# Optimization experiments

Measured on AMD Instinct MI355X. Metric: run time of the kernel, lower is better.

Reference implementation:

```python
import jax, jax.numpy as jnp
import numpy as np

D_MODEL = 256
SCALE = 1.0 / float(np.sqrt(D_MODEL))


def setup_inputs() -> dict:
    key = jax.random.key(0)
    kq, kk, kv, km = jax.random.split(key, 4)
    B, S, D = 16, 2048, D_MODEL
    q = jax.random.normal(kq, (B, S, D), dtype=jnp.float32)
    k = jax.random.normal(kk, (B, S, D), dtype=jnp.float32)
    v = jax.random.normal(kv, (B, S, D), dtype=jnp.float32)
    mask = jax.random.randint(km, (1, S, S), 0, 2, dtype=jnp.int32)
    return {"q": q, "k": k, "v": v, "mask": mask}


def reference(q, k, v, mask):
    # scores: [B, S, S] = q @ k^T * scale
    scores = jnp.einsum("bqd,bkd->bqk", q, k) * SCALE
    scores = jnp.where(mask == 0, -jnp.inf, scores)
    attn_weights = jax.nn.softmax(scores, axis=-1)
    output = jnp.einsum("bqk,bkd->bqd", attn_weights, v)
    return (output, attn_weights)
```

## Files before the change

kernel.cpp:

```cpp
#include <hip/hip_runtime.h>
#include <hip/hip_bf16.h>
#include <stdint.h>


#define B_ 16
#define S_ 2048
#define D_ 256
#define SCALE_ 0.0625f

typedef __attribute__((ext_vector_type(8))) short bf16x8;
typedef __attribute__((ext_vector_type(4))) float f32x4;

__device__ __forceinline__ uint16_t f2bf(float f) {
  uint32_t u = __float_as_uint(f);
  u += 0x7fffu + ((u >> 16) & 1u);
  return (uint16_t)(u >> 16);
}

__global__ void k_convert(const float* __restrict__ src, uint16_t* __restrict__ dst) {
  const int t = blockIdx.x * blockDim.x + threadIdx.x;
  const float4* s = (const float4*)src + (size_t)t * 2;
  float4 a = s[0], b = s[1];
  ushort4 lo = { f2bf(a.x), f2bf(a.y), f2bf(a.z), f2bf(a.w) };
  ushort4 hi = { f2bf(b.x), f2bf(b.y), f2bf(b.z), f2bf(b.w) };
  ((ushort4*)dst)[(size_t)t * 2]     = lo;
  ((ushort4*)dst)[(size_t)t * 2 + 1] = hi;
}

__global__ void k_transpose(const float* __restrict__ V, uint16_t* __restrict__ Vt) {
  __shared__ float tile[64][68];
  const int b = blockIdx.z, kv0 = blockIdx.x * 64, d0 = blockIdx.y * 64;
  const int t = threadIdx.x;
  {
    const int r = t >> 2, c = (t & 3) * 16;
    const float4* src = (const float4*)(V + ((size_t)b * S_ + kv0 + r) * D_ + d0 + c);
    float4 x0 = src[0], x1 = src[1], x2 = src[2], x3 = src[3];
    *(float4*)&tile[r][c]      = x0;
    *(float4*)&tile[r][c + 4]  = x1;
    *(float4*)&tile[r][c + 8]  = x2;
    *(float4*)&tile[r][c + 12] = x3;
  }
  __syncthreads();
  {
    const int dl = t >> 2, c = (t & 3) * 16;
    uint16_t o[16];
#pragma unroll
    for (int i = 0; i < 16; ++i) o[i] = f2bf(tile[c + i][dl]);
    uint16_t* dst = Vt + ((size_t)b * D_ + d0 + dl) * S_ + kv0 + c;
#pragma unroll
    for (int i = 0; i < 4; ++i) {
      ushort4 v4 = { o[4*i], o[4*i+1], o[4*i+2], o[4*i+3] };
      *(ushort4*)(dst + 4*i) = v4;
    }
  }
}

__global__ void k_maskpack(const int* __restrict__ mask, unsigned long long* __restrict__ Mb) {
  const int wid  = blockIdx.x * 4 + (threadIdx.x >> 6);
  const int lane = threadIdx.x & 63;
  const int row = wid >> 5, w64 = wid & 31;
  const int m = mask[(size_t)row * S_ + w64 * 64 + lane];
  unsigned long long bits = __ballot(m != 0);
  if (lane == 0) Mb[row * 32 + w64] = bits;
}

__global__ __launch_bounds__(512, 2) void k_attn(
    const float* __restrict__ Q, const uint16_t* __restrict__ Kb,
    const unsigned long long* __restrict__ Mb, float* __restrict__ attn) {
  __shared__ uint16_t Ks[128 * 256];
  const int b = blockIdx.y, q0 = blockIdx.x * 128;
  const int tid = threadIdx.x, w = tid >> 6, lane = tid & 63;
  const int wq = w >> 1, wkv = w & 1;
  const int l15 = lane & 15, lq = lane >> 4;
  const int qbase = q0 + wq * 32;

  bf16x8 aq[2][8];
#pragma unroll
  for (int qt = 0; qt < 2; ++qt) {
    const float* qrow = Q + ((size_t)b * S_ + qbase + qt * 16 + l15) * D_;
#pragma unroll
    for (int dc = 0; dc < 8; ++dc) {
      const float4* p = (const float4*)(qrow + dc * 32 + lq * 8);
      float4 x = p[0], y = p[1];
      union { bf16x8 v; uint16_t u[8]; } fr;
      fr.u[0] = f2bf(x.x); fr.u[1] = f2bf(x.y); fr.u[2] = f2bf(x.z); fr.u[3] = f2bf(x.w);
      fr.u[4] = f2bf(y.x); fr.u[5] = f2bf(y.y); fr.u[6] = f2bf(y.z); fr.u[7] = f2bf(y.w);
      aq[qt][dc] = fr.v;
    }
  }

  float rowpart[2][4] = {{0.f,0.f,0.f,0.f},{0.f,0.f,0.f,0.f}};
  float inv_[2][4];

  for (int pass = 0; pass < 2; ++pass) {
    for (int kvt = 0; kvt < 16; ++kvt) {
      const int kvb = kvt * 128;
      {
        const uint4* src = (const uint4*)(Kb + ((size_t)b * S_ + kvb) * D_);
#pragma unroll
        for (int i = 0; i < 8; ++i) {
          const int g = i * 512 + tid;
          const int row = g >> 5, gcol = g & 31;
          uint4 val = src[row * 32 + gcol];
          const int gs = (gcol & ~7) | ((gcol ^ row) & 7);
          *(uint4*)&Ks[(row * 32 + gs) * 8] = val;
        }
      }
      __syncthreads();

      f32x4 acc[2][4];
#pragma unroll
      for (int qt = 0; qt < 2; ++qt)
#pragma unroll
        for (int kt = 0; kt < 4; ++kt) acc[qt][kt] = 0.f;

#pragma unroll
      for (int dc = 0; dc < 8; ++dc) {
        bf16x8 bk[4];
#pragma unroll
        for (int kt = 0; kt < 4; ++kt) {
          const int kvl = wkv * 64 + kt * 16 + l15;
          const int g = dc * 4 + lq;
          const int gs = (g & ~7) | ((g ^ kvl) & 7);
          bk[kt] = *(const bf16x8*)&Ks[(kvl * 32 + gs) * 8];
        }
#pragma unroll
        for (int qt = 0; qt < 2; ++qt)
#pragma unroll
          for (int kt = 0; kt < 4; ++kt)
            acc[qt][kt] = __builtin_amdgcn_mfma_f32_16x16x32_bf16(
                aq[qt][dc], bk[kt], acc[qt][kt], 0, 0, 0);
      }

#pragma unroll
      for (int qt = 0; qt < 2; ++qt) {
#pragma unroll
        for (int r = 0; r < 4; ++r) {
          const int row = qbase + qt * 16 + lq * 4 + r;
          const unsigned long long mw = Mb[row * 32 + kvt * 2 + wkv];
#pragma unroll
          for (int kt = 0; kt < 4; ++kt) {
            const float s = acc[qt][kt][r] * SCALE_;
            const int bit = kt * 16 + l15;
            const float e = ((mw >> bit) & 1ull) ? __expf(s) : 0.0f;
            if (pass == 0) {
              rowpart[qt][r] += e;
            } else {
              attn[(size_t)b * S_ * S_ + (size_t)row * S_ +
                   kvb + wkv * 64 + kt * 16 + l15] = e * inv_[qt][r];
            }
          }
        }
      }
      __syncthreads();
    }

    if (pass == 0) {
#pragma unroll
      for (int qt = 0; qt < 2; ++qt)
#pragma unroll
        for (int r = 0; r < 4; ++r) {
          float v = rowpart[qt][r];
          v += __shfl_xor(v, 1); v += __shfl_xor(v, 2);
          v += __shfl_xor(v, 4); v += __shfl_xor(v, 8);
          rowpart[qt][r] = v;
        }
      float* red = (float*)(void*)Ks;
      if (l15 == 0) {
#pragma unroll
        for (int qt = 0; qt < 2; ++qt)
#pragma unroll
          for (int r = 0; r < 4; ++r) {
            const int rl = wq * 32 + qt * 16 + lq * 4 + r;
            red[wkv * 128 + rl] = rowpart[qt][r];
          }
      }
      __syncthreads();
#pragma unroll
      for (int qt = 0; qt < 2; ++qt)
#pragma unroll
        for (int r = 0; r < 4; ++r) {
          const int rl = wq * 32 + qt * 16 + lq * 4 + r;
          inv_[qt][r] = 1.0f / (red[rl] + red[128 + rl]);
        }
      __syncthreads();
    }
  }
}

__global__ __launch_bounds__(512, 2) void k_out(
    const float* __restrict__ attn, const uint16_t* __restrict__ Vt,
    float* __restrict__ O) {
  __shared__ uint16_t As[128 * 64];
  __shared__ uint16_t Vs[256 * 64];
  const int b = blockIdx.y, q0 = blockIdx.x * 128;
  const int tid = threadIdx.x, w = tid >> 6, lane = tid & 63;
  const int wq = w >> 2, wd = w & 3;
  const int l15 = lane & 15, lq = lane >> 4;

  f32x4 acc[4][4];
#pragma unroll
  for (int qt = 0; qt < 4; ++qt)
#pragma unroll
    for (int dt = 0; dt < 4; ++dt) acc[qt][dt] = 0.f;

  for (int kvt = 0; kvt < 32; ++kvt) {
    const int kvb = kvt * 64;
    {
      const int row = tid >> 2, gc = (tid & 3) * 2;
      const float4* ap = (const float4*)(attn + ((size_t)b * S_ + q0 + row) * S_ + kvb + (tid & 3) * 16);
      float4 a0 = ap[0], a1 = ap[1], a2 = ap[2], a3 = ap[3];
      union { uint4 u; uint16_t s[8]; } g0, g1;
      g0.s[0] = f2bf(a0.x); g0.s[1] = f2bf(a0.y); g0.s[2] = f2bf(a0.z); g0.s[3] = f2bf(a0.w);
      g0.s[4] = f2bf(a1.x); g0.s[5] = f2bf(a1.y); g0.s[6] = f2bf(a1.z); g0.s[7] = f2bf(a1.w);
      g1.s[0] = f2bf(a2.x); g1.s[1] = f2bf(a2.y); g1.s[2] = f2bf(a2.z); g1.s[3] = f2bf(a2.w);
      g1.s[4] = f2bf(a3.x); g1.s[5] = f2bf(a3.y); g1.s[6] = f2bf(a3.z); g1.s[7] = f2bf(a3.w);
      *(uint4*)&As[(row * 8 + (gc ^ (row & 7))) * 8]       = g0.u;
      *(uint4*)&As[(row * 8 + ((gc + 1) ^ (row & 7))) * 8] = g1.u;
    }
    {
      const int d = tid >> 1, gc = (tid & 1) * 4;
      const uint4* vp = (const uint4*)(Vt + ((size_t)b * D_ + d) * S_ + kvb + (tid & 1) * 32);
#pragma unroll
      for (int i = 0; i < 4; ++i) {
        uint4 vv = vp[i];
        *(uint4*)&Vs[(d * 8 + ((gc + i) ^ (d & 7))) * 8] = vv;
      }
    }
    __syncthreads();

#pragma unroll
    for (int kc = 0; kc < 2; ++kc) {
      bf16x8 af[4], bv[4];
      const int g = kc * 4 + lq;
#pragma unroll
      for (int qt = 0; qt < 4; ++qt) {
        const int ql = wq * 64 + qt * 16 + l15;
        af[qt] = *(const bf16x8*)&As[(ql * 8 + (g ^ (ql & 7))) * 8];
      }
#pragma unroll
      for (int dt = 0; dt < 4; ++dt) {
        const int dl = wd * 64 + dt * 16 + l15;
        bv[dt] = *(const bf16x8*)&Vs[(dl * 8 + (g ^ (dl & 7))) * 8];
      }
#pragma unroll
      for (int qt = 0; qt < 4; ++qt)
#pragma unroll
        for (int dt = 0; dt < 4; ++dt)
          acc[qt][dt] = __builtin_amdgcn_mfma_f32_16x16x32_bf16(af[qt], bv[dt], acc[qt][dt], 0, 0, 0);
    }
    __syncthreads();
  }

#pragma unroll
  for (int qt = 0; qt < 4; ++qt)
#pragma unroll
    for (int dt = 0; dt < 4; ++dt)
#pragma unroll
      for (int r = 0; r < 4; ++r)
        O[((size_t)b * S_ + q0 + wq * 64 + qt * 16 + lq * 4 + r) * D_ +
          wd * 64 + dt * 16 + l15] = acc[qt][dt][r];
}

extern "C" void kernel_launch(void* const* d_in, const int* in_sizes, int n_in,
                              void* d_out, int out_size, void* d_ws, size_t ws_size,
                              hipStream_t stream) {
  const float* q = (const float*)d_in[0];
  const float* k = (const float*)d_in[1];
  const float* v = (const float*)d_in[2];
  const int* mask = (const int*)d_in[3];

  float* out  = (float*)d_out;
  float* attn = out + (size_t)B_ * S_ * D_;

  uint16_t* Kb = (uint16_t*)d_ws;
  uint16_t* Vt = Kb + (size_t)B_ * S_ * D_;
  unsigned long long* Mb = (unsigned long long*)(Vt + (size_t)B_ * S_ * D_);

  k_convert<<<dim3(2048), dim3(512), 0, stream>>>(k, Kb);
  k_transpose<<<dim3(32, 4, 16), dim3(256), 0, stream>>>(v, Vt);
  k_maskpack<<<dim3(16384), dim3(256), 0, stream>>>(mask, Mb);
  k_attn<<<dim3(16, 16), dim3(512), 0, stream>>>(q, Kb, Mb, attn);
  k_out<<<dim3(16, 16), dim3(512), 0, stream>>>(attn, Vt, out);
}
```

Measured before the change: 636.4 us.

## Single-pass softmax storing unnormalized exps, normalize in output kernel, async LDS loads

The attention kernel no longer runs QK^T twice. It writes unnormalized masked exponentials plus per-row inverse sums in one pass, and the output kernel rescales the attention matrix in place (read-modify-write) while converting it to bf16 for the PV matmul. K and V tiles are now loaded straight into LDS with global_load_lds, and both kernels move to 256-thread blocks over 64 query rows, which doubles the grid. This removes half the QK matmul work, but k_out now rewrites the full fp32 attention matrix, which adds memory traffic.

```diff
diff --git a/kernel.cpp b/kernel.cpp
--- a/kernel.cpp
+++ b/kernel.cpp
@@ -15,6 +15,12 @@
   uint32_t u = __float_as_uint(f);
   u += 0x7fffu + ((u >> 16) & 1u);
   return (uint16_t)(u >> 16);
+}
+
+typedef __attribute__((address_space(3))) uint32_t lds_u32;
+typedef __attribute__((address_space(1))) const uint32_t glb_u32;
+__device__ __forceinline__ void gload_lds16(const void* g, void* l) {
+  __builtin_amdgcn_global_load_lds((glb_u32*)g, (lds_u32*)l, 16, 0, 0);
 }
 
 __global__ void k_convert(const float* __restrict__ src, uint16_t* __restrict__ dst) {
@@ -64,11 +70,12 @@
   if (lane == 0) Mb[row * 32 + w64] = bits;
 }
 
-__global__ __launch_bounds__(512, 2) void k_attn(
+__global__ __launch_bounds__(256, 2) void k_attn(
     const float* __restrict__ Q, const uint16_t* __restrict__ Kb,
-    const unsigned long long* __restrict__ Mb, float* __restrict__ attn) {
+    const unsigned long long* __restrict__ Mb,
+    float* __restrict__ E, float* __restrict__ Winv) {
   __shared__ uint16_t Ks[128 * 256];
-  const int b = blockIdx.y, q0 = blockIdx.x * 128;
+  const int b = blockIdx.y, q0 = blockIdx.x * 64;
   const int tid = threadIdx.x, w = tid >> 6, lane = tid & 63;
   const int wq = w >> 1, wkv = w & 1;
   const int l15 = lane & 15, lq = lane >> 4;
@@ -90,113 +97,107 @@
   }
 
   float rowpart[2][4] = {{0.f,0.f,0.f,0.f},{0.f,0.f,0.f,0.f}};
-  float inv_[2][4];
-
-  for (int pass = 0; pass < 2; ++pass) {
-    for (int kvt = 0; kvt < 16; ++kvt) {
-      const int kvb = kvt * 128;
-      {
-        const uint4* src = (const uint4*)(Kb + ((size_t)b * S_ + kvb) * D_);
-#pragma unroll
-        for (int i = 0; i < 8; ++i) {
-          const int g = i * 512 + tid;
-          const int row = g >> 5, gcol = g & 31;
-          uint4 val = src[row * 32 + gcol];
-          const int gs = (gcol & ~7) | ((gcol ^ row) & 7);
-          *(uint4*)&Ks[(row * 32 + gs) * 8] = val;
+
+  for (int kvt = 0; kvt < 16; ++kvt) {
+    const int kvb = kvt * 128;
+    __syncthreads();
+    {
+      const uint16_t* tbase = Kb + ((size_t)b * S_ + kvb) * D_;
+#pragma unroll
+      for (int it = 0; it < 16; ++it) {
+        const int s = (it * 4 + w) * 64 + lane;
+        const int r = s >> 5, c = s & 31;
+        const int g = (c & ~7) | ((c ^ r) & 7);
+        gload_lds16(tbase + (size_t)r * D_ + g * 8, &Ks[(it * 4 + w) * 64 * 8]);
+      }
+    }
+    __syncthreads();
+
+    f32x4 acc[2][4];
+#pragma unroll
+    for (int qt = 0; qt < 2; ++qt)
+#pragma unroll
+      for (int kt = 0; kt < 4; ++kt) acc[qt][kt] = 0.f;
+
+#pragma unroll
+    for (int dc = 0; dc < 8; ++dc) {
+      bf16x8 bk[4];
+#pragma unroll
+      for (int kt = 0; kt < 4; ++kt) {
+        const int kvl = wkv * 64 + kt * 16 + l15;
+        const int g = dc * 4 + lq;
+        const int gs = (g & ~7) | ((g ^ kvl) & 7);
+        bk[kt] = *(const bf16x8*)&Ks[(kvl * 32 + gs) * 8];
+      }
+#pragma unroll
+      for (int qt = 0; qt < 2; ++qt)
+#pragma unroll
+        for (int kt = 0; kt < 4; ++kt)
+          acc[qt][kt] = __builtin_amdgcn_mfma_f32_16x16x32_bf16(
+              aq[qt][dc], bk[kt], acc[qt][kt], 0, 0, 0);
+    }
+
+#pragma unroll
+    for (int qt = 0; qt < 2; ++qt) {
+#pragma unroll
+      for (int r = 0; r < 4; ++r) {
+        const int row = qbase + qt * 16 + lq * 4 + r;
+        const unsigned long long mw = Mb[row * 32 + kvt * 2 + wkv];
+        float* erow = E + (size_t)b * S_ * S_ + (size_t)row * S_ + kvb + wkv * 64 + l15;
+#pragma unroll
+        for (int kt = 0; kt < 4; ++kt) {
+          const float sc = acc[qt][kt][r] * SCALE_;
+          const int bit = kt * 16 + l15;
+          const float e = ((mw >> bit) & 1ull) ? __expf(sc) : 0.0f;
+          rowpart[qt][r] += e;
+          erow[kt * 16] = e;
         }
       }
-      __syncthreads();
-
-      f32x4 acc[2][4];
-#pragma unroll
-      for (int qt = 0; qt < 2; ++qt)
-#pragma unroll
-        for (int kt = 0; kt < 4; ++kt) acc[qt][kt] = 0.f;
-
-#pragma unroll
-      for (int dc = 0; dc < 8; ++dc) {
-        bf16x8 bk[4];
-#pragma unroll
-        for (int kt = 0; kt < 4; ++kt) {
-          const int kvl = wkv * 64 + kt * 16 + l15;
-          const int g = dc * 4 + lq;
-          const int gs = (g & ~7) | ((g ^ kvl) & 7);
-          bk[kt] = *(const bf16x8*)&Ks[(kvl * 32 + gs) * 8];
-        }
-#pragma unroll
-        for (int qt = 0; qt < 2; ++qt)
-#pragma unroll
-          for (int kt = 0; kt < 4; ++kt)
-            acc[qt][kt] = __builtin_amdgcn_mfma_f32_16x16x32_bf16(
-                aq[qt][dc], bk[kt], acc[qt][kt], 0, 0, 0);
-      }
-
-#pragma unroll
-      for (int qt = 0; qt < 2; ++qt) {
-#pragma unroll
-        for (int r = 0; r < 4; ++r) {
-          const int row = qbase + qt * 16 + lq * 4 + r;
-          const unsigned long long mw = Mb[row * 32 + kvt * 2 + wkv];
-#pragma unroll
-          for (int kt = 0; kt < 4; ++kt) {
-            const float s = acc[qt][kt][r] * SCALE_;
-            const int bit = kt * 16 + l15;
-            const float e = ((mw >> bit) & 1ull) ? __expf(s) : 0.0f;
-            if (pass == 0) {
-              rowpart[qt][r] += e;
-            } else {
-              attn[(size_t)b * S_ * S_ + (size_t)row * S_ +
-                   kvb + wkv * 64 + kt * 16 + l15] = e * inv_[qt][r];
-            }
-          }
-        }
-      }
-      __syncthreads();
-    }
-
-    if (pass == 0) {
-#pragma unroll
-      for (int qt = 0; qt < 2; ++qt)
-#pragma unroll
-        for (int r = 0; r < 4; ++r) {
-          float v = rowpart[qt][r];
-          v += __shfl_xor(v, 1); v += __shfl_xor(v, 2);
-          v += __shfl_xor(v, 4); v += __shfl_xor(v, 8);
-          rowpart[qt][r] = v;
-        }
-      float* red = (float*)(void*)Ks;
-      if (l15 == 0) {
-#pragma unroll
-        for (int qt = 0; qt < 2; ++qt)
-#pragma unroll
-          for (int r = 0; r < 4; ++r) {
-            const int rl = wq * 32 + qt * 16 + lq * 4 + r;
-            red[wkv * 128 + rl] = rowpart[qt][r];
-          }
-      }
-      __syncthreads();
-#pragma unroll
-      for (int qt = 0; qt < 2; ++qt)
-#pragma unroll
-        for (int r = 0; r < 4; ++r) {
-          const int rl = wq * 32 + qt * 16 + lq * 4 + r;
-          inv_[qt][r] = 1.0f / (red[rl] + red[128 + rl]);
-        }
-      __syncthreads();
-    }
-  }
-}
-
-__global__ __launch_bounds__(512, 2) void k_out(
-    const float* __restrict__ attn, const uint16_t* __restrict__ Vt,
-    float* __restrict__ O) {
-  __shared__ uint16_t As[128 * 64];
+    }
+  }
+
+#pragma unroll
+  for (int qt = 0; qt < 2; ++qt)
+#pragma unroll
+    for (int r = 0; r < 4; ++r) {
+      float v = rowpart[qt][r];
+      v += __shfl_xor(v, 1); v += __shfl_xor(v, 2);
+      v += __shfl_xor(v, 4); v += __shfl_xor(v, 8);
+      rowpart[qt][r] = v;
+    }
+  __syncthreads();
+  float* red = (float*)(void*)Ks;
+  if (l15 == 0) {
+#pragma unroll
+    for (int qt = 0; qt < 2; ++qt)
+#pragma unroll
+      for (int r = 0; r < 4; ++r) {
+        const int rl = wq * 32 + qt * 16 + lq * 4 + r;
+        red[wkv * 64 + rl] = rowpart[qt][r];
+      }
+  }
+  __syncthreads();
+  if (wkv == 0 && l15 == 0) {
+#pragma unroll
+    for (int qt = 0; qt < 2; ++qt)
+#pragma unroll
+      for (int r = 0; r < 4; ++r) {
+        const int rl = wq * 32 + qt * 16 + lq * 4 + r;
+        Winv[(size_t)b * S_ + q0 + rl] = 1.0f / (red[rl] + red[64 + rl]);
+      }
+  }
+}
+
+__global__ __launch_bounds__(256, 2) void k_out(
+    float* __restrict__ attn, const uint16_t* __restrict__ Vt,
+    const float* __restrict__ Winv, float* __restrict__ O) {
+  __shared__ uint16_t As[64 * 64];
   __shared__ uint16_t Vs[256 * 64];
-  const int b = blockIdx.y, q0 = blockIdx.x * 128;
+  const int b = blockIdx.y, q0 = blockIdx.x * 64;
   const int tid = threadIdx.x, w = tid >> 6, lane = tid & 63;
-  const int wq = w >> 2, wd = w & 3;
   const int l15 = lane & 15, lq = lane >> 4;
+  const int srow = tid >> 2, scol = (tid & 3) * 16;
+  const float inv_r = Winv[(size_t)b * S_ + q0 + srow];
 
   f32x4 acc[4][4];
 #pragma unroll
@@ -206,26 +207,35 @@
 
   for (int kvt = 0; kvt < 32; ++kvt) {
     const int kvb = kvt * 64;
+    __syncthreads();
     {
-      const int row = tid >> 2, gc = (tid & 3) * 2;
-      const float4* ap = (const float4*)(attn + ((size_t)b * S_ + q0 + row) * S_ + kvb + (tid & 3) * 16);
-      float4 a0 = ap[0], a1 = ap[1], a2 = ap[2], a3 = ap[3];
-      union { uint4 u; uint16_t s[8]; } g0, g1;
-      g0.s[0] = f2bf(a0.x); g0.s[1] = f2bf(a0.y); g0.s[2] = f2bf(a0.z); g0.s[3] = f2bf(a0.w);
-      g0.s[4] = f2bf(a1.x); g0.s[5] = f2bf(a1.y); g0.s[6] = f2bf(a1.z); g0.s[7] = f2bf(a1.w);
-      g1.s[0] = f2bf(a2.x); g1.s[1] = f2bf(a2.y); g1.s[2] = f2bf(a2.z); g1.s[3] = f2bf(a2.w);
-      g1.s[4] = f2bf(a3.x); g1.s[5] = f2bf(a3.y); g1.s[6] = f2bf(a3.z); g1.s[7] = f2bf(a3.w);
-      *(uint4*)&As[(row * 8 + (gc ^ (row & 7))) * 8]       = g0.u;
-      *(uint4*)&As[(row * 8 + ((gc + 1) ^ (row & 7))) * 8] = g1.u;
+      const uint16_t* tbase = Vt + (size_t)b * D_ * S_ + kvb;
+#pragma unroll
+      for (int it = 0; it < 8; ++it) {
+        const int s = (it * 4 + w) * 64 + lane;
+        const int d = s >> 3, c = s & 7;
+        const int g = c ^ (d & 7);
+        gload_lds16(tbase + (size_t)d * S_ + g * 8, &Vs[(it * 4 + w) * 64 * 8]);
+      }
     }
     {
-      const int d = tid >> 1, gc = (tid & 1) * 4;
-      const uint4* vp = (const uint4*)(Vt + ((size_t)b * D_ + d) * S_ + kvb + (tid & 1) * 32);
-#pragma unroll
-      for (int i = 0; i < 4; ++i) {
-        uint4 vv = vp[i];
-        *(uint4*)&Vs[(d * 8 + ((gc + i) ^ (d & 7))) * 8] = vv;
-      }
+      float* ap = attn + ((size_t)b * S_ + q0 + srow) * S_ + kvb + scol;
+      float4 a0 = ((const float4*)ap)[0], a1 = ((const float4*)ap)[1];
+      float4 a2 = ((const float4*)ap)[2], a3 = ((const float4*)ap)[3];
+      a0.x *= inv_r; a0.y *= inv_r; a0.z *= inv_r; a0.w *= inv_r;
+      a1.x *= inv_r; a1.y *= inv_r; a1.z *= inv_r; a1.w *= inv_r;
+      a2.x *= inv_r; a2.y *= inv_r; a2.z *= inv_r; a2.w *= inv_r;
+      a3.x *= inv_r; a3.y *= inv_r; a3.z *= inv_r; a3.w *= inv_r;
+      ((float4*)ap)[0] = a0; ((float4*)ap)[1] = a1;
+      ((float4*)ap)[2] = a2; ((float4*)ap)[3] = a3;
+      union { uint4 u; uint16_t h[8]; } g0, g1;
+      g0.h[0] = f2bf(a0.x); g0.h[1] = f2bf(a0.y); g0.h[2] = f2bf(a0.z); g0.h[3] = f2bf(a0.w);
+      g0.h[4] = f2bf(a1.x); g0.h[5] = f2bf(a1.y); g0.h[6] = f2bf(a1.z); g0.h[7] = f2bf(a1.w);
+      g1.h[0] = f2bf(a2.x); g1.h[1] = f2bf(a2.y); g1.h[2] = f2bf(a2.z); g1.h[3] = f2bf(a2.w);
+      g1.h[4] = f2bf(a3.x); g1.h[5] = f2bf(a3.y); g1.h[6] = f2bf(a3.z); g1.h[7] = f2bf(a3.w);
+      const int gc = (tid & 3) * 2;
+      *(uint4*)&As[(srow * 8 + (gc ^ (srow & 7))) * 8]       = g0.u;
+      *(uint4*)&As[(srow * 8 + ((gc + 1) ^ (srow & 7))) * 8] = g1.u;
     }
     __syncthreads();
 
@@ -235,12 +245,12 @@
       const int g = kc * 4 + lq;
 #pragma unroll
       for (int qt = 0; qt < 4; ++qt) {
-        const int ql = wq * 64 + qt * 16 + l15;
+        const int ql = qt * 16 + l15;
         af[qt] = *(const bf16x8*)&As[(ql * 8 + (g ^ (ql & 7))) * 8];
       }
 #pragma unroll
       for (int dt = 0; dt < 4; ++dt) {
-        const int dl = wd * 64 + dt * 16 + l15;
+        const int dl = w * 64 + dt * 16 + l15;
         bv[dt] = *(const bf16x8*)&Vs[(dl * 8 + (g ^ (dl & 7))) * 8];
       }
 #pragma unroll
@@ -249,7 +259,6 @@
         for (int dt = 0; dt < 4; ++dt)
           acc[qt][dt] = __builtin_amdgcn_mfma_f32_16x16x32_bf16(af[qt], bv[dt], acc[qt][dt], 0, 0, 0);
     }
-    __syncthreads();
   }
 
 #pragma unroll
@@ -258,8 +267,8 @@
     for (int dt = 0; dt < 4; ++dt)
 #pragma unroll
       for (int r = 0; r < 4; ++r)
-        O[((size_t)b * S_ + q0 + wq * 64 + qt * 16 + lq * 4 + r) * D_ +
-          wd * 64 + dt * 16 + l15] = acc[qt][dt][r];
+        O[((size_t)b * S_ + q0 + qt * 16 + lq * 4 + r) * D_ +
+          w * 64 + dt * 16 + l15] = acc[qt][dt][r];
 }
 
 extern "C" void kernel_launch(void* const* d_in, const int* in_sizes, int n_in,
@@ -276,10 +285,11 @@
   uint16_t* Kb = (uint16_t*)d_ws;
   uint16_t* Vt = Kb + (size_t)B_ * S_ * D_;
   unsigned long long* Mb = (unsigned long long*)(Vt + (size_t)B_ * S_ * D_);
+  float* Winv = (float*)(Mb + (size_t)S_ * 32);
 
   k_convert<<<dim3(2048), dim3(512), 0, stream>>>(k, Kb);
   k_transpose<<<dim3(32, 4, 16), dim3(256), 0, stream>>>(v, Vt);
   k_maskpack<<<dim3(16384), dim3(256), 0, stream>>>(mask, Mb);
-  k_attn<<<dim3(16, 16), dim3(512), 0, stream>>>(q, Kb, Mb, attn);
-  k_out<<<dim3(16, 16), dim3(512), 0, stream>>>(attn, Vt, out);
-}
+  k_attn<<<dim3(32, 16), dim3(256), 0, stream>>>(q, Kb, Mb, attn, Winv);
+  k_out<<<dim3(32, 16), dim3(256), 0, stream>>>(attn, Vt, Winv, out);
+}
```

Result: faster. 579.4 us (-9.0%).
